# Kernel tuning notes

Measured on AMD Instinct MI355X. Metric: run time of the kernel, lower is better.

## Reference

```python
import jax, jax.numpy as jnp
import numpy as np

ACT_GUARD = 2.0   # 2 ** act_guard_bit (act_guard_bit = 1)
WGT_GUARD = 2.0   # 2 ** weight_guard_bit (weight_guard_bit = 1)


def _ste_round(v):
    # straight-through estimator round (QNMethod.STE)
    return v + jax.lax.stop_gradient(jnp.round(v) - v)


def setup_inputs() -> dict:
    key = jax.random.key(0)
    k_x, k_w, k_b = jax.random.split(key, 3)
    B, S, DIN, DOUT = 4, 2048, 2048, 8192
    ACT_INIT_S, ACT_INIT_Q, LOG_S_INIT = -10.0, 10.0, -8.0
    x = jax.random.normal(k_x, (B, S, DIN), dtype=jnp.float32)
    weight = jax.random.normal(k_w, (DOUT, DIN), dtype=jnp.float32) * 0.02
    bias = jax.random.normal(k_b, (DOUT,), dtype=jnp.float32) * 0.01
    log_act_s = jnp.full((1,), ACT_INIT_S, dtype=jnp.float32)
    log_act_q = jnp.full((1,), ACT_INIT_Q, dtype=jnp.float32)
    act_b = jnp.full((1,), -jnp.exp2(ACT_INIT_Q - 1.0), dtype=jnp.float32)  # -512
    log_wght_s = jnp.full((DOUT, 1), LOG_S_INIT, dtype=jnp.float32)
    return {"x": x, "weight": weight, "bias": bias, "log_act_s": log_act_s,
            "log_act_q": log_act_q, "act_b": act_b, "log_wght_s": log_wght_s}


def reference(x, weight, bias, log_act_s, log_act_q, act_b, log_wght_s):
    # --- activation fake-quant (per-tensor) ---
    s = jnp.exp2(log_act_s)                       # [1]
    q = jnp.exp2(log_act_q)                       # [1]
    zp = jnp.round(act_b / s * ACT_GUARD) / ACT_GUARD * s  # guard-bit rounded zero point
    lo, hi = zp, zp + q - s
    qx = _ste_round((jnp.clip(x, lo, hi) - zp) / s)
    x_dq = qx * s + zp                            # dequantized activations

    # --- weight fake-quant (per-channel over out dim, amin/amax over dim 1) ---
    w_scale = jnp.exp2(log_wght_s)                # [DOUT, 1]
    wmin = jnp.min(weight, axis=1, keepdims=True)
    wmax = jnp.max(weight, axis=1, keepdims=True)
    qwmin = jnp.round(wmin / w_scale * WGT_GUARD) / WGT_GUARD * w_scale
    qwmax = jnp.round(wmax / w_scale * WGT_GUARD) / WGT_GUARD * w_scale
    qw = _ste_round((jnp.clip(weight, qwmin, qwmax) - qwmin) / w_scale)
    w_dq = qw * w_scale + qwmin                   # dequantized weights

    # --- affine: y = x @ W.T + b ---
    return jnp.einsum('bsi,oi->bso', x_dq, w_dq) + bias
```

## Files before the change

kernel.cpp:

```cpp
#include <hip/hip_runtime.h>
#include <hip/hip_bf16.h>


using f16x8 = __attribute__((ext_vector_type(8))) _Float16;
using f32x4 = __attribute__((ext_vector_type(4))) float;

#define AS1 __attribute__((address_space(1)))
#define AS3 __attribute__((address_space(3)))

static __device__ __forceinline__ void gload_lds16(const void* g, void* l) {
    __builtin_amdgcn_global_load_lds((const AS1 void*)g, (AS3 void*)l, 16, 0, 0);
}

__global__ __launch_bounds__(256) void quant_kernel(
    const float* __restrict__ X,
    const float* __restrict__ las, const float* __restrict__ laq,
    const float* __restrict__ ab,
    const float* __restrict__ W, const float* __restrict__ lws,
    _Float16* __restrict__ Xq, _Float16* __restrict__ Wq) {
    constexpr int K = 2048;
    __shared__ float smn[4], smx[4];
    const int t = threadIdx.x;

    if (blockIdx.x < 8192) {
        const float ls = las[0], lq = laq[0];
        const float s = exp2f(ls);
        const float rs = exp2f(-ls);
        const float q = exp2f(lq);
        const float zp = rintf(ab[0] * rs * 2.0f) * 0.5f * s;
        const float lo = zp;
        const float hi = (zp + q) - s;

        const size_t base = ((size_t)blockIdx.x * 256 + t) * 8;
        float4 v0 = *(const float4*)&X[base];
        float4 v1 = *(const float4*)&X[base + 4];
        float vals[8] = {v0.x, v0.y, v0.z, v0.w, v1.x, v1.y, v1.z, v1.w};

        f16x8 out;
#pragma unroll
        for (int i = 0; i < 8; ++i) {
            float c = fminf(fmaxf(vals[i], lo), hi);
            float qx = rintf((c - zp) * rs);
            out[i] = (_Float16)(qx * s + zp);
        }
        *(f16x8*)&Xq[base] = out;
    } else {
        const int row = blockIdx.x - 8192;
        const float* w = W + (size_t)row * K;

        float4 v0 = ((const float4*)w)[t * 2];
        float4 v1 = ((const float4*)w)[t * 2 + 1];
        float vals[8] = {v0.x, v0.y, v0.z, v0.w, v1.x, v1.y, v1.z, v1.w};

        float mn = vals[0], mx = vals[0];
#pragma unroll
        for (int i = 1; i < 8; ++i) {
            mn = fminf(mn, vals[i]);
            mx = fmaxf(mx, vals[i]);
        }
#pragma unroll
        for (int off = 32; off >= 1; off >>= 1) {
            mn = fminf(mn, __shfl_xor(mn, off));
            mx = fmaxf(mx, __shfl_xor(mx, off));
        }
        if ((t & 63) == 0) { smn[t >> 6] = mn; smx[t >> 6] = mx; }
        __syncthreads();
        mn = fminf(fminf(smn[0], smn[1]), fminf(smn[2], smn[3]));
        mx = fmaxf(fmaxf(smx[0], smx[1]), fmaxf(smx[2], smx[3]));

        const float l = lws[row];
        const float ws = exp2f(l);
        const float rs = exp2f(-l);
        const float qwmin = rintf(mn * rs * 2.0f) * 0.5f * ws;
        const float qwmax = rintf(mx * rs * 2.0f) * 0.5f * ws;

        f16x8 out;
#pragma unroll
        for (int i = 0; i < 8; ++i) {
            float c = fminf(fmaxf(vals[i], qwmin), qwmax);
            float qw = rintf((c - qwmin) * rs);
            out[i] = (_Float16)(qw * ws + qwmin);
        }
        *(f16x8*)&Wq[(size_t)row * K + (size_t)t * 8] = out;
    }
}

__global__ __launch_bounds__(512, 2) void gemm_kernel(
    const _Float16* __restrict__ A, const _Float16* __restrict__ B,
    const float* __restrict__ bias, float* __restrict__ C) {
    constexpr int N = 8192, K = 2048;
    constexpr int KT = K / 64;

    __shared__ char smem[131072];

    const int bid = blockIdx.x;
    const int j = bid >> 3;
    const int bm = (bid & 7) * 4 + (j & 3);
    const int bn = j >> 2;

    const int t = threadIdx.x;
    const int lane = t & 63;
    const int wid = t >> 6;
    const int wr = wid >> 2;
    const int wc = wid & 3;
    const int l15 = lane & 15;
    const int lq = lane >> 4;

    const int d0 = t * 16, d1 = d0 + 8192;
    const int r0 = d0 >> 7, c0 = (((d0 & 127) ^ (((d0 >> 7) & 7) << 4)) >> 1);
    const int r1 = d1 >> 7, c1 = (((d1 & 127) ^ (((d1 >> 7) & 7) << 4)) >> 1);
    const _Float16* Agb = A + (size_t)bm * 256 * K;
    const _Float16* Bgb = B + (size_t)bn * 256 * K;

    const int cp0 = (lq * 16) ^ ((l15 & 7) << 4);
    const int cp1 = cp0 ^ 64;

    f32x4 acc[8][4] = {};
    f16x8 fA0[4][2], fA1[4][2], fB0[2][2], fB1[2][2];

#define STAGE(GB, RO, DBS, H, KS) do {                                         \
        const _Float16* _g = (GB) + (size_t)((H) * 128) * K + (size_t)(KS) * 64;\
        char* _l = smem + (RO) + ((DBS) * 2 + (H)) * 16384;                    \
        gload_lds16(_g + (size_t)r0 * K + c0, _l + d0);                        \
        gload_lds16(_g + (size_t)r1 * K + c1, _l + d1);                        \
    } while (0)

#define LDAF(dst, DBv, MLO) do {                                               \
        const char* _s = smem + ((DBv) * 2 + wr) * 16384 + l15 * 128;          \
        _Pragma("unroll")                                                      \
        for (int _m = 0; _m < 4; ++_m) {                                       \
            dst[_m][0] = *(const f16x8*)(_s + ((MLO) + _m) * 2048 + cp0);      \
            dst[_m][1] = *(const f16x8*)(_s + ((MLO) + _m) * 2048 + cp1);      \
        }                                                                      \
    } while (0)

#define LDBF(dst, DBv, NLO) do {                                               \
        const char* _s = smem + 65536 + ((DBv) * 2 + (wc >> 1)) * 16384 +      \
                         (wc & 1) * 8192 + l15 * 128;                          \
        _Pragma("unroll")                                                      \
        for (int _n = 0; _n < 2; ++_n) {                                       \
            dst[_n][0] = *(const f16x8*)(_s + ((NLO) + _n) * 2048 + cp0);      \
            dst[_n][1] = *(const f16x8*)(_s + ((NLO) + _n) * 2048 + cp1);      \
        }                                                                      \
    } while (0)

#define QMFMA(MLO, NLO, AF, BF) do {                                           \
        _Pragma("unroll")                                                      \
        for (int _m = 0; _m < 4; ++_m)                                         \
            _Pragma("unroll")                                                  \
            for (int _n = 0; _n < 2; ++_n) {                                   \
                f32x4 _c = acc[(MLO) + _m][(NLO) + _n];                        \
                _c = __builtin_amdgcn_mfma_f32_16x16x32_f16(                   \
                    AF[_m][0], BF[_n][0], _c, 0, 0, 0);                        \
                _c = __builtin_amdgcn_mfma_f32_16x16x32_f16(                   \
                    AF[_m][1], BF[_n][1], _c, 0, 0, 0);                        \
                acc[(MLO) + _m][(NLO) + _n] = _c;                              \
            }                                                                  \
    } while (0)

#define HALFITER(DBv, S1, S2, S3, S4, VMW) do {                                \
                                                          \
        LDAF(fA0, DBv, 0); LDBF(fB0, DBv, 0);                                  \
        S1;                                                                    \
        asm volatile("s_waitcnt lgkmcnt(8)");                                  \
        __builtin_amdgcn_s_barrier();                                          \
        asm volatile("s_waitcnt lgkmcnt(0)");                                  \
        __builtin_amdgcn_s_setprio(1);                                         \
        QMFMA(0, 0, fA0, fB0);                                                 \
        __builtin_amdgcn_s_setprio(0);                                         \
        __builtin_amdgcn_s_barrier();                                          \
                                                           \
        LDBF(fB1, DBv, 2);                                                     \
        S2;                                                                    \
        __builtin_amdgcn_s_barrier();                                          \
        asm volatile("s_waitcnt lgkmcnt(0)");                                  \
        __builtin_amdgcn_s_setprio(1);                                         \
        QMFMA(0, 2, fA0, fB1);                                                 \
        __builtin_amdgcn_s_setprio(0);                                         \
        __builtin_amdgcn_s_barrier();                                          \
                                                           \
        LDAF(fA1, DBv, 4);                                                     \
        S3;                                                                    \
        __builtin_amdgcn_s_barrier();                                          \
        asm volatile("s_waitcnt lgkmcnt(0)");                                  \
        __builtin_amdgcn_s_setprio(1);                                         \
        QMFMA(4, 2, fA1, fB1);                                                 \
        __builtin_amdgcn_s_setprio(0);                                         \
        __builtin_amdgcn_s_barrier();                                          \
                                                           \
        S4;                                                                    \
        __builtin_amdgcn_s_barrier();                                          \
        __builtin_amdgcn_s_setprio(1);                                         \
        QMFMA(4, 0, fA1, fB0);                                                 \
        __builtin_amdgcn_s_setprio(0);                                         \
        asm volatile("s_waitcnt vmcnt(" #VMW ")" ::: "memory");                \
        __builtin_amdgcn_s_barrier();                                          \
    } while (0)

    STAGE(Bgb, 65536, 0, 0, 0);
    STAGE(Agb, 0,     0, 0, 0);
    STAGE(Agb, 0,     0, 1, 0);
    STAGE(Bgb, 65536, 0, 1, 0);
    STAGE(Bgb, 65536, 1, 0, 1);
    STAGE(Bgb, 65536, 1, 1, 1);
    asm volatile("s_waitcnt vmcnt(4)" ::: "memory");
    __builtin_amdgcn_s_barrier();

    for (int it = 0; it < KT / 2; ++it) {
        const int b  = 2 * it + 1;
        const int aN = (2 * it + 2 < KT) ? 2 * it + 2 : KT - 2;
        const int bN = (2 * it + 3 < KT) ? 2 * it + 3 : KT - 1;

        HALFITER(0,
                 STAGE(Agb, 0,     1, 0, b),
                 STAGE(Agb, 0,     1, 1, b),
                 STAGE(Bgb, 65536, 0, 0, aN),
                 STAGE(Agb, 0,     0, 0, aN), 4);
        HALFITER(1,
                 STAGE(Agb, 0,     0, 1, aN),
                 STAGE(Bgb, 65536, 0, 1, aN),
                 STAGE(Bgb, 65536, 1, 0, bN),
                 STAGE(Bgb, 65536, 1, 1, bN), 4);
    }
#undef HALFITER
#undef QMFMA
#undef LDBF
#undef LDAF
#undef STAGE

#pragma unroll
    for (int m = 0; m < 8; ++m) {
        const int row = bm * 256 + wr * 128 + m * 16 + lq * 4;
#pragma unroll
        for (int n = 0; n < 4; ++n) {
            const int col = bn * 256 + wc * 64 + n * 16 + l15;
            const float bv = bias[col];
#pragma unroll
            for (int r = 0; r < 4; ++r) {
                C[(size_t)(row + r) * N + col] = acc[m][n][r] + bv;
            }
        }
    }
}

extern "C" void kernel_launch(void* const* d_in, const int* in_sizes, int n_in,
                              void* d_out, int out_size, void* d_ws, size_t ws_size,
                              hipStream_t stream) {
    const float* x    = (const float*)d_in[0];
    const float* w    = (const float*)d_in[1];
    const float* bias = (const float*)d_in[2];
    const float* las  = (const float*)d_in[3];
    const float* laq  = (const float*)d_in[4];
    const float* ab   = (const float*)d_in[5];
    const float* lws  = (const float*)d_in[6];
    float* out = (float*)d_out;

    constexpr size_t MK = (size_t)8192 * 2048;
    _Float16* xq = (_Float16*)d_ws;
    _Float16* wq = (_Float16*)((char*)d_ws + MK * sizeof(_Float16));

    quant_kernel<<<16384, 256, 0, stream>>>(x, las, laq, ab, w, lws, xq, wq);
    gemm_kernel<<<1024, 512, 0, stream>>>(xq, wq, bias, out);
}
```

Before: 278.9 us.

## Load B fragments directly from global into registers, halve LDS to A only

Replaces the LDS-staged B tile with per-wave direct global loads of B fragments into double-buffered registers, so LDS holds only the A tile and shrinks from 128KB to 64KB. The pipeline is restructured into two-phase tiles with full vmcnt(0) waits each tile. This removes the LDS writes and reads for B but loses the sharing of B between waves: each B row is loaded by both row-waves straight from global/L2. The loads are 16-byte per lane with row stride K, so coalescing is poor, and the full vmcnt drain serializes the prefetch.

```diff
diff --git a/kernel.cpp b/kernel.cpp
--- a/kernel.cpp
+++ b/kernel.cpp
@@ -91,7 +91,7 @@
     constexpr int N = 8192, K = 2048;
     constexpr int KT = K / 64;
 
-    __shared__ char smem[131072];
+    __shared__ char smem[65536];
 
     const int bid = blockIdx.x;
     const int j = bid >> 3;
@@ -110,123 +110,97 @@
     const int r0 = d0 >> 7, c0 = (((d0 & 127) ^ (((d0 >> 7) & 7) << 4)) >> 1);
     const int r1 = d1 >> 7, c1 = (((d1 & 127) ^ (((d1 >> 7) & 7) << 4)) >> 1);
     const _Float16* Agb = A + (size_t)bm * 256 * K;
-    const _Float16* Bgb = B + (size_t)bn * 256 * K;
+    const _Float16* Bw = B + (size_t)(bn * 256 + wc * 64 + l15) * K + lq * 8;
 
     const int cp0 = (lq * 16) ^ ((l15 & 7) << 4);
     const int cp1 = cp0 ^ 64;
 
     f32x4 acc[8][4] = {};
-    f16x8 fA0[4][2], fA1[4][2], fB0[2][2], fB1[2][2];
-
-#define STAGE(GB, RO, DBS, H, KS) do {                                         \
-        const _Float16* _g = (GB) + (size_t)((H) * 128) * K + (size_t)(KS) * 64;\
-        char* _l = smem + (RO) + ((DBS) * 2 + (H)) * 16384;                    \
+    f16x8 fA[4][2], fBa[4][2], fBb[4][2];
+
+#define STAGEH(DBS, H, KS) do {                                                \
+        const _Float16* _g = Agb + (size_t)((H) * 128) * K + (size_t)(KS) * 64;\
+        char* _l = smem + ((DBS) * 2 + (H)) * 16384;                           \
         gload_lds16(_g + (size_t)r0 * K + c0, _l + d0);                        \
         gload_lds16(_g + (size_t)r1 * K + c1, _l + d1);                        \
     } while (0)
 
-#define LDAF(dst, DBv, MLO) do {                                               \
+#define LDAF(DBv, MLO) do {                                                    \
         const char* _s = smem + ((DBv) * 2 + wr) * 16384 + l15 * 128;          \
         _Pragma("unroll")                                                      \
         for (int _m = 0; _m < 4; ++_m) {                                       \
-            dst[_m][0] = *(const f16x8*)(_s + ((MLO) + _m) * 2048 + cp0);      \
-            dst[_m][1] = *(const f16x8*)(_s + ((MLO) + _m) * 2048 + cp1);      \
+            fA[_m][0] = *(const f16x8*)(_s + ((MLO) + _m) * 2048 + cp0);       \
+            fA[_m][1] = *(const f16x8*)(_s + ((MLO) + _m) * 2048 + cp1);       \
         }                                                                      \
     } while (0)
 
-#define LDBF(dst, DBv, NLO) do {                                               \
-        const char* _s = smem + 65536 + ((DBv) * 2 + (wc >> 1)) * 16384 +      \
-                         (wc & 1) * 8192 + l15 * 128;                          \
+#define LOADB(FB, KS) do {                                                     \
         _Pragma("unroll")                                                      \
-        for (int _n = 0; _n < 2; ++_n) {                                       \
-            dst[_n][0] = *(const f16x8*)(_s + ((NLO) + _n) * 2048 + cp0);      \
-            dst[_n][1] = *(const f16x8*)(_s + ((NLO) + _n) * 2048 + cp1);      \
+        for (int _n = 0; _n < 4; ++_n) {                                       \
+            FB[_n][0] = *(const f16x8*)(Bw + (size_t)_n * 16 * K + (KS) * 64); \
+            FB[_n][1] = *(const f16x8*)(Bw + (size_t)_n * 16 * K + (KS) * 64 + 32);\
         }                                                                      \
     } while (0)
 
-#define QMFMA(MLO, NLO, AF, BF) do {                                           \
+#define HMFMA(MLO, FB) do {                                                    \
         _Pragma("unroll")                                                      \
         for (int _m = 0; _m < 4; ++_m)                                         \
             _Pragma("unroll")                                                  \
-            for (int _n = 0; _n < 2; ++_n) {                                   \
-                f32x4 _c = acc[(MLO) + _m][(NLO) + _n];                        \
+            for (int _n = 0; _n < 4; ++_n) {                                   \
+                f32x4 _c = acc[(MLO) + _m][_n];                                \
                 _c = __builtin_amdgcn_mfma_f32_16x16x32_f16(                   \
-                    AF[_m][0], BF[_n][0], _c, 0, 0, 0);                        \
+                    fA[_m][0], FB[_n][0], _c, 0, 0, 0);                        \
                 _c = __builtin_amdgcn_mfma_f32_16x16x32_f16(                   \
-                    AF[_m][1], BF[_n][1], _c, 0, 0, 0);                        \
-                acc[(MLO) + _m][(NLO) + _n] = _c;                              \
+                    fA[_m][1], FB[_n][1], _c, 0, 0, 0);                        \
+                acc[(MLO) + _m][_n] = _c;                                      \
             }                                                                  \
     } while (0)
 
-#define HALFITER(DBv, S1, S2, S3, S4, VMW) do {                                \
-                                                          \
-        LDAF(fA0, DBv, 0); LDBF(fB0, DBv, 0);                                  \
-        S1;                                                                    \
-        asm volatile("s_waitcnt lgkmcnt(8)");                                  \
-        __builtin_amdgcn_s_barrier();                                          \
-        asm volatile("s_waitcnt lgkmcnt(0)");                                  \
-        __builtin_amdgcn_s_setprio(1);                                         \
-        QMFMA(0, 0, fA0, fB0);                                                 \
-        __builtin_amdgcn_s_setprio(0);                                         \
-        __builtin_amdgcn_s_barrier();                                          \
-                                                           \
-        LDBF(fB1, DBv, 2);                                                     \
-        S2;                                                                    \
-        __builtin_amdgcn_s_barrier();                                          \
-        asm volatile("s_waitcnt lgkmcnt(0)");                                  \
-        __builtin_amdgcn_s_setprio(1);                                         \
-        QMFMA(0, 2, fA0, fB1);                                                 \
-        __builtin_amdgcn_s_setprio(0);                                         \
-        __builtin_amdgcn_s_barrier();                                          \
-                                                           \
-        LDAF(fA1, DBv, 4);                                                     \
-        S3;                                                                    \
-        __builtin_amdgcn_s_barrier();                                          \
-        asm volatile("s_waitcnt lgkmcnt(0)");                                  \
-        __builtin_amdgcn_s_setprio(1);                                         \
-        QMFMA(4, 2, fA1, fB1);                                                 \
-        __builtin_amdgcn_s_setprio(0);                                         \
-        __builtin_amdgcn_s_barrier();                                          \
-                                                           \
-        S4;                                                                    \
-        __builtin_amdgcn_s_barrier();                                          \
-        __builtin_amdgcn_s_setprio(1);                                         \
-        QMFMA(4, 0, fA1, fB0);                                                 \
-        __builtin_amdgcn_s_setprio(0);                                         \
-        asm volatile("s_waitcnt vmcnt(" #VMW ")" ::: "memory");                \
-        __builtin_amdgcn_s_barrier();                                          \
-    } while (0)
-
-    STAGE(Bgb, 65536, 0, 0, 0);
-    STAGE(Agb, 0,     0, 0, 0);
-    STAGE(Agb, 0,     0, 1, 0);
-    STAGE(Bgb, 65536, 0, 1, 0);
-    STAGE(Bgb, 65536, 1, 0, 1);
-    STAGE(Bgb, 65536, 1, 1, 1);
-    asm volatile("s_waitcnt vmcnt(4)" ::: "memory");
-    __builtin_amdgcn_s_barrier();
+#define VMC0()  asm volatile("s_waitcnt vmcnt(0)" ::: "memory")
+#define LG0()   asm volatile("s_waitcnt lgkmcnt(0)")
+#define BAR()   __builtin_amdgcn_s_barrier()
+#define PRIO(P) __builtin_amdgcn_s_setprio(P)
+
+#define TILE(DBv, NXT, FBC, FBN) do {                                          \
+                                                                      \
+        LDAF(DBv, 0);                                                          \
+        STAGEH((DBv) ^ 1, 0, NXT);                                             \
+        LOADB(FBN, NXT);                                                       \
+        BAR();                                                                 \
+        LG0();                                                                 \
+        PRIO(1); HMFMA(0, FBC); PRIO(0);                                       \
+        BAR();                                                                 \
+                                                                      \
+        LDAF(DBv, 4);                                                          \
+        STAGEH((DBv) ^ 1, 1, NXT);                                             \
+        BAR();                                                                 \
+        LG0();                                                                 \
+        PRIO(1); HMFMA(4, FBC); PRIO(0);                                       \
+        VMC0();                                                                \
+        BAR();                                                                 \
+    } while (0)
+
+    STAGEH(0, 0, 0);
+    STAGEH(0, 1, 0);
+    LOADB(fBa, 0);
+    VMC0();
+    BAR();
 
     for (int it = 0; it < KT / 2; ++it) {
-        const int b  = 2 * it + 1;
-        const int aN = (2 * it + 2 < KT) ? 2 * it + 2 : KT - 2;
-        const int bN = (2 * it + 3 < KT) ? 2 * it + 3 : KT - 1;
-
-        HALFITER(0,
-                 STAGE(Agb, 0,     1, 0, b),
-                 STAGE(Agb, 0,     1, 1, b),
-                 STAGE(Bgb, 65536, 0, 0, aN),
-                 STAGE(Agb, 0,     0, 0, aN), 4);
-        HALFITER(1,
-                 STAGE(Agb, 0,     0, 1, aN),
-                 STAGE(Bgb, 65536, 0, 1, aN),
-                 STAGE(Bgb, 65536, 1, 0, bN),
-                 STAGE(Bgb, 65536, 1, 1, bN), 4);
+        const int n1 = (2 * it + 1 < KT) ? 2 * it + 1 : KT - 1;
+        const int n2 = (2 * it + 2 < KT) ? 2 * it + 2 : KT - 1;
+        TILE(0, n1, fBa, fBb);
+        TILE(1, n2, fBb, fBa);
     }
-#undef HALFITER
-#undef QMFMA
-#undef LDBF
+#undef TILE
+#undef HMFMA
+#undef LOADB
 #undef LDAF
-#undef STAGE
+#undef STAGEH
+#undef VMC0
+#undef LG0
+#undef BAR
+#undef PRIO
 
 #pragma unroll
     for (int m = 0; m < 8; ++m) {
```

New measurement: 437.1 us. +56.7%, slower.
